# Optimization experiments

Measured on AMD Instinct MI355X. Metric: run time of the kernel, lower is better.

## Reference

```python
import jax, jax.numpy as jnp
from jax import lax
import numpy as np


def conv2d(x, w, b=None, stride=1, padding=0, groups=1, dilation=1):
    out = lax.conv_general_dilated(
        x, w, (stride, stride), [(padding, padding)] * 2,
        rhs_dilation=(dilation, dilation), feature_group_count=groups,
        dimension_numbers=('NCHW', 'OIHW', 'NCHW'))
    return out if b is None else out + b[None, :, None, None]


def unfold1d(x, k, axis):
    # torch.nn.functional.unfold with kernel (k,1) or (1,k), pad k//2 on that axis.
    # Returns [B, C, k, H, W] (channel-major, kernel-tap inner), matching torch layout.
    pad = k // 2
    pads = [(0, 0)] * 4
    pads[axis] = (pad, pad)
    xp = jnp.pad(x, pads)
    return jnp.stack([lax.slice_in_dim(xp, i, i + x.shape[axis], axis=axis)
                      for i in range(k)], axis=2)


def ikba(x, att, k, g, b_cb, w_cb):
    # Per-pixel dynamic grouped conv: attention mixes nset codebook kernels,
    # applied as vertical (k,1) then horizontal (1,k) unfold-matmul-fold.
    B, c, H, W = x.shape
    nset = att.shape[1]
    cg = c // g
    P = H * W
    a = att.reshape(B, nset, P).transpose(0, 2, 1)          # [B,P,nset]
    bias = a @ b_cb[0]                                      # [B,P,c]
    attk = a @ w_cb[0]                                      # [B,P, 2*c*cg*k]
    half = attk.shape[-1] // 2
    ah = attk[..., :half].reshape(B, P, g, cg, cg * k)
    aw = attk[..., half:].reshape(B, P, g, cg, cg * k)
    # vertical pass
    ufh = unfold1d(x, k, 2).reshape(B, g, cg * k, P).transpose(0, 3, 1, 2)  # [B,P,g,cg*k]
    xh = jnp.einsum('bpgij,bpgj->bpgi', ah, ufh).reshape(B, P, c)
    xh = xh.transpose(0, 2, 1).reshape(B, c, H, W)
    # horizontal pass
    ufw = unfold1d(xh, k, 3).reshape(B, g, cg * k, P).transpose(0, 3, 1, 2)
    xw = jnp.einsum('bpgij,bpgj->bpgi', aw, ufw).reshape(B, P, c) + bias
    return xw.transpose(0, 2, 1).reshape(B, c, H, W)


def hff_forward(x, dw1_w, dw2_w, proj_w, lka0_w, lkas_w, lka1_w, lka1_b,
                sca_w, sca_b, c1a_w, c1b_w, c2a_w, c2a_b, c2b_w, c2b_b,
                c211_w, c211_b, w_cb, b_cb, attgamma, ga1):
    C = x.shape[1]
    K, GC = 3, 4
    g = C // GC
    sca = conv2d(jnp.mean(x, axis=(2, 3), keepdims=True), sca_w, sca_b)
    x1 = conv2d(conv2d(x, dw1_w), dw2_w, padding=1, groups=C)
    lka = conv2d(conv2d(conv2d(x, lka0_w, padding=2, groups=C),
                        lkas_w, padding=9, groups=C, dilation=3), lka1_w, lka1_b)
    t = conv2d(x, c2a_w, c2a_b, padding=1, groups=c2a_w.shape[0])
    t1, t2 = jnp.split(t, 2, axis=1)  # SimpleGate
    att = conv2d(t1 * t2, c2b_w, c2b_b) * attgamma + conv2d(x, c211_w, c211_b)
    uf = conv2d(conv2d(x, c1a_w), c1b_w, padding=1, groups=C)
    x2 = ikba(uf, att, K, g, b_cb, w_cb) * ga1 + uf
    return conv2d(x1 * x2 * sca * lka, proj_w)


def setup_inputs() -> dict:
    key = jax.random.key(0)
    ks = jax.random.split(key, 24)
    B, C, H, W = 2, 256, 64, 64
    nset, k, gc = 128, 3, 4
    g = C // gc
    cg = C // g
    def rn(i, shape, scale=0.02):
        return jax.random.normal(ks[i], shape, jnp.float32) * scale
    return {
        'x': jax.random.normal(ks[0], (B, C, H, W), jnp.float32),
        'dw1_w': rn(1, (C, C, 1, 1)),
        'dw2_w': rn(2, (C, 1, 3, 3), 0.1),
        'proj_w': rn(3, (C, C, 1, 1)),
        'lka0_w': rn(4, (C, 1, 5, 5), 0.1),
        'lkas_w': rn(5, (C, 1, 7, 7), 0.1),
        'lka1_w': rn(6, (C, C, 1, 1)),
        'lka1_b': rn(7, (C,)),
        'sca_w': rn(8, (C, C, 1, 1)),
        'sca_b': rn(9, (C,)),
        'c1a_w': rn(10, (C, C, 1, 1)),
        'c1b_w': rn(11, (C, 1, 3, 3), 0.1),
        'c2a_w': rn(12, (32, C // 32, 3, 3), 0.1),
        'c2a_b': rn(13, (32,)),
        'c2b_w': rn(14, (nset, 16, 1, 1), 0.1),
        'c2b_b': rn(15, (nset,)),
        'c211_w': rn(16, (nset, C, 1, 1)),
        'c211_b': rn(17, (nset,)),
        'w_cb': rn(18, (1, nset, C * cg * k * 2), 0.05),
        'b_cb': rn(19, (1, nset, C), 0.05),
        'attgamma': jnp.full((1, nset, 1, 1), 0.01, jnp.float32),
        'ga1': jnp.full((1, C, 1, 1), 0.01, jnp.float32),
    }


def reference(x, dw1_w, dw2_w, proj_w, lka0_w, lkas_w, lka1_w, lka1_b,
              sca_w, sca_b, c1a_w, c1b_w, c2a_w, c2a_b, c2b_w, c2b_b,
              c211_w, c211_b, w_cb, b_cb, attgamma, ga1):
    return hff_forward(x, dw1_w, dw2_w, proj_w, lka0_w, lkas_w, lka1_w, lka1_b,
                       sca_w, sca_b, c1a_w, c1b_w, c2a_w, c2a_b, c2b_w, c2b_b,
                       c211_w, c211_b, w_cb, b_cb, attgamma, ga1)
```

## Files before the change

### kernel.cpp

```cpp
#include <hip/hip_runtime.h>
#include <cstddef>

#define P_ 4096
#define HW_ 64

typedef __bf16 bf16x8 __attribute__((ext_vector_type(8)));
typedef float f32x4 __attribute__((ext_vector_type(4)));

__device__ inline ushort f2bf(float f) {
  unsigned u = __float_as_uint(f);
  unsigned r = (u + 0x7FFFu + ((u >> 16) & 1u)) >> 16;
  return (ushort)r;
}
__device__ inline float bf2f(ushort h) {
  return __uint_as_float(((unsigned)h) << 16);
}
__device__ inline unsigned pack2(ushort a, ushort b) {
  return (unsigned)a | ((unsigned)b << 16);
}

__global__ __launch_bounds__(256) void prep_mean_kernel(
    const float* __restrict__ w_cb, const float* __restrict__ dw1_w,
    const float* __restrict__ lka1_w, const float* __restrict__ c1a_w,
    const float* __restrict__ proj_w, const float* __restrict__ c211_w,
    const float* __restrict__ b_cb, ushort* __restrict__ wT,
    ushort* __restrict__ W5h, ushort* __restrict__ W5l,
    ushort* __restrict__ bth, ushort* __restrict__ btl,
    const float* __restrict__ x, float* __restrict__ mean) {
  __shared__ float T[128][65];
  int blk = blockIdx.x;
  int t = threadIdx.x;
  if (blk < 96) {
    int c0 = blk * 64;
#pragma unroll
    for (int i = 0; i < 32; ++i) {
      int l = i * 256 + t;
      int n = l >> 6, c = l & 63;
      T[n][c] = w_cb[(size_t)n * 6144 + c0 + c];
    }
    __syncthreads();
#pragma unroll
    for (int i = 0; i < 4; ++i) {
      int l = i * 256 + t;
      int c = l >> 4, n8 = (l & 15) << 3;
      ushort v[8];
#pragma unroll
      for (int u = 0; u < 8; ++u) v[u] = f2bf(T[n8 + u][c]);
      *(uint4*)&wT[(size_t)(c0 + c) * 128 + n8] = *(uint4*)v;
    }
  } else if (blk < 240) {
    int f = (blk - 96) * 2048 + t * 8;
    const float* srcs[5] = {dw1_w, lka1_w, c1a_w, proj_w, c211_w};
    const int base[6] = {0, 65536, 131072, 196608, 262144, 294912};
    int r = 0;
    while (f >= base[r + 1]) ++r;
    const float* s = srcs[r] + (f - base[r]);
    float4 a = *(const float4*)s;
    float4 b4 = *(const float4*)(s + 4);
    float vv[8] = {a.x, a.y, a.z, a.w, b4.x, b4.y, b4.z, b4.w};
    ushort vh[8], vl[8];
#pragma unroll
    for (int u = 0; u < 8; ++u) {
      ushort h = f2bf(vv[u]);
      vh[u] = h;
      vl[u] = f2bf(vv[u] - bf2f(h));
    }
    *(uint4*)&W5h[f] = *(uint4*)vh;
    *(uint4*)&W5l[f] = *(uint4*)vl;
  } else if (blk < 244) {
    int c0 = (blk - 240) * 64;
#pragma unroll
    for (int i = 0; i < 32; ++i) {
      int l = i * 256 + t;
      int n = l >> 6, c = l & 63;
      T[n][c] = b_cb[(size_t)n * 256 + c0 + c];
    }
    __syncthreads();
#pragma unroll
    for (int i = 0; i < 4; ++i) {
      int l = i * 256 + t;
      int c = l >> 4, n8 = (l & 15) << 3;
      ushort vh[8], vl[8];
#pragma unroll
      for (int u = 0; u < 8; ++u) {
        float fv = T[n8 + u][c];
        ushort h = f2bf(fv);
        vh[u] = h;
        vl[u] = f2bf(fv - bf2f(h));
      }
      *(uint4*)&bth[(size_t)(c0 + c) * 128 + n8] = *(uint4*)vh;
      *(uint4*)&btl[(size_t)(c0 + c) * 128 + n8] = *(uint4*)vl;
    }
  } else {
    int bc = blk - 244;
    const float* xp = x + (size_t)bc * P_;
    float s = 0.f;
    for (int i = t; i < P_; i += 256) s += xp[i];
    float* red = (float*)T;
    red[t] = s;
    __syncthreads();
    for (int off2 = 128; off2 > 0; off2 >>= 1) {
      if (t < off2) red[t] += red[t + off2];
      __syncthreads();
    }
    if (t == 0) mean[bc] = red[0] * (1.f / P_);
  }
}

__global__ __launch_bounds__(256) void sca_xsplit_kernel(
    const float* __restrict__ x, ushort* __restrict__ dh,
    ushort* __restrict__ dl, const float* __restrict__ mean,
    const float* __restrict__ w, const float* __restrict__ bias,
    float* __restrict__ sca) {
  __shared__ float T[128][65];
  int blk = blockIdx.x;
  int t = threadIdx.x;
  if (blk < 256) {
    const int K = 256;
    int p0 = (blk & 63) * 64;
    int kb = (blk >> 6) & 1;
    int b = blk >> 7;
    const float* sb = x + ((size_t)b * K + kb * 128) * P_;
    ushort* dhb = dh + (size_t)b * P_ * K + (size_t)kb * 128;
    ushort* dlb = dl + (size_t)b * P_ * K + (size_t)kb * 128;
#pragma unroll
    for (int i = 0; i < 32; ++i) {
      int l = i * 256 + t;
      int n = l >> 6, c = l & 63;
      T[n][c] = sb[(size_t)n * P_ + p0 + c];
    }
    __syncthreads();
#pragma unroll
    for (int i = 0; i < 4; ++i) {
      int l = i * 256 + t;
      int c = l >> 4, n8 = (l & 15) << 3;
      ushort vh[8], vl[8];
#pragma unroll
      for (int u = 0; u < 8; ++u) {
        float f = T[n8 + u][c];
        ushort h = f2bf(f);
        vh[u] = h;
        vl[u] = f2bf(f - bf2f(h));
      }
      *(uint4*)&dhb[(size_t)(p0 + c) * K + n8] = *(uint4*)vh;
      *(uint4*)&dlb[(size_t)(p0 + c) * K + n8] = *(uint4*)vl;
    }
  } else {
    int b = blk - 256, c = t;
    const float* mb = mean + b * 256;
    const float* wr = w + c * 256;
    float s = bias[c];
    for (int k = 0; k < 256; ++k) s += wr[k] * mb[k];
    sca[b * 256 + c] = s;
  }
}

__global__ __launch_bounds__(256) void xsplit_kernel(
    const float* __restrict__ src, ushort* __restrict__ dh,
    ushort* __restrict__ dl, int K) {
  int p0 = blockIdx.x * 64;
  int kb = blockIdx.y;
  int b = blockIdx.z;
  const float* sb = src + ((size_t)b * K + kb * 128) * P_;
  ushort* dhb = dh + (size_t)b * P_ * K + (size_t)kb * 128;
  ushort* dlb = dl + (size_t)b * P_ * K + (size_t)kb * 128;
  __shared__ float T[128][65];
  int t = threadIdx.x;
#pragma unroll
  for (int i = 0; i < 32; ++i) {
    int l = i * 256 + t;
    int n = l >> 6, c = l & 63;
    T[n][c] = sb[(size_t)n * P_ + p0 + c];
  }
  __syncthreads();
#pragma unroll
  for (int i = 0; i < 4; ++i) {
    int l = i * 256 + t;
    int c = l >> 4, n8 = (l & 15) << 3;
    ushort vh[8], vl[8];
#pragma unroll
    for (int u = 0; u < 8; ++u) {
      float f = T[n8 + u][c];
      ushort h = f2bf(f);
      vh[u] = h;
      vl[u] = f2bf(f - bf2f(h));
    }
    *(uint4*)&dhb[(size_t)(p0 + c) * K + n8] = *(uint4*)vh;
    *(uint4*)&dlb[(size_t)(p0 + c) * K + n8] = *(uint4*)vl;
  }
}

__global__ __launch_bounds__(256) void gemm_bf16s_kernel(
    const ushort* __restrict__ Wh, const ushort* __restrict__ Wl,
    const ushort* __restrict__ Xh, const ushort* __restrict__ Xl,
    const float* __restrict__ bias, float* __restrict__ out, int M, int K) {
  int p0 = blockIdx.x * 64, m0 = blockIdx.y * 64, b = blockIdx.z;
  __shared__ __align__(16) ushort Wsh[64 * 72];
  __shared__ __align__(16) ushort Wsl[64 * 72];
  __shared__ __align__(16) ushort Xsh[64 * 72];
  __shared__ __align__(16) ushort Xsl[64 * 72];
  int t = threadIdx.x;
  int w = t >> 6, lane = t & 63, lm = lane & 15, lq = lane >> 4;
  f32x4 C[4];
#pragma unroll
  for (int pt = 0; pt < 4; ++pt) C[pt] = (f32x4)(0.f);
  const ushort* Whb = Wh + (size_t)m0 * K;
  const ushort* Wlb = Wl + (size_t)m0 * K;
  const ushort* Xhb = Xh + ((size_t)b * P_ + p0) * K;
  const ushort* Xlb = Xl + ((size_t)b * P_ + p0) * K;
  for (int k0 = 0; k0 < K; k0 += 64) {
#pragma unroll
    for (int i = 0; i < 2; ++i) {
      int u = i * 256 + t;
      int row = u >> 3, k8 = (u & 7) * 8;
      *(uint4*)&Wsh[row * 72 + k8] = *(const uint4*)&Whb[(size_t)row * K + k0 + k8];
      *(uint4*)&Wsl[row * 72 + k8] = *(const uint4*)&Wlb[(size_t)row * K + k0 + k8];
      *(uint4*)&Xsh[row * 72 + k8] = *(const uint4*)&Xhb[(size_t)row * K + k0 + k8];
      *(uint4*)&Xsl[row * 72 + k8] = *(const uint4*)&Xlb[(size_t)row * K + k0 + k8];
    }
    __syncthreads();
#pragma unroll
    for (int kt = 0; kt < 2; ++kt) {
      bf16x8 Ah = *(const bf16x8*)&Wsh[(w * 16 + lm) * 72 + kt * 32 + lq * 8];
      bf16x8 Al = *(const bf16x8*)&Wsl[(w * 16 + lm) * 72 + kt * 32 + lq * 8];
#pragma unroll
      for (int pt = 0; pt < 4; ++pt) {
        bf16x8 Bh = *(const bf16x8*)&Xsh[(pt * 16 + lm) * 72 + kt * 32 + lq * 8];
        bf16x8 Bl = *(const bf16x8*)&Xsl[(pt * 16 + lm) * 72 + kt * 32 + lq * 8];
        C[pt] = __builtin_amdgcn_mfma_f32_16x16x32_bf16(Ah, Bh, C[pt], 0, 0, 0);
        C[pt] = __builtin_amdgcn_mfma_f32_16x16x32_bf16(Al, Bh, C[pt], 0, 0, 0);
        C[pt] = __builtin_amdgcn_mfma_f32_16x16x32_bf16(Ah, Bl, C[pt], 0, 0, 0);
      }
    }
    __syncthreads();
  }
#pragma unroll
  for (int pt = 0; pt < 4; ++pt) {
    int p = p0 + pt * 16 + lm;
#pragma unroll
    for (int r = 0; r < 4; ++r) {
      int m = m0 + w * 16 + lq * 4 + r;
      float v = C[pt][r];
      if (bias) v += bias[m];
      out[((size_t)b * M + m) * P_ + p] = v;
    }
  }
}

__global__ __launch_bounds__(256) void gemm3_kernel(
    const ushort* __restrict__ Xh, const ushort* __restrict__ Xl,
    const ushort* __restrict__ W5h, const ushort* __restrict__ W5l,
    const float* __restrict__ c211_b, float* __restrict__ B1,
    float* __restrict__ B3, float* __restrict__ att0) {
  const int K = 256;
  int my = blockIdx.y;
  const ushort *Wh, *Wl;
  float* out;
  const float* bias = nullptr;
  int M, m0;
  if (my < 4) {
    Wh = W5h; Wl = W5l; out = B1; M = 256; m0 = my * 64;
  } else if (my < 8) {
    Wh = W5h + 131072; Wl = W5l + 131072; out = B3; M = 256; m0 = (my - 4) * 64;
  } else {
    Wh = W5h + 262144; Wl = W5l + 262144; out = att0; M = 128;
    m0 = (my - 8) * 64; bias = c211_b;
  }
  int p0 = blockIdx.x * 64, b = blockIdx.z;
  __shared__ __align__(16) ushort Wsh[64 * 72];
  __shared__ __align__(16) ushort Wsl[64 * 72];
  __shared__ __align__(16) ushort Xsh[64 * 72];
  __shared__ __align__(16) ushort Xsl[64 * 72];
  int t = threadIdx.x;
  int w = t >> 6, lane = t & 63, lm = lane & 15, lq = lane >> 4;
  f32x4 C[4];
#pragma unroll
  for (int pt = 0; pt < 4; ++pt) C[pt] = (f32x4)(0.f);
  const ushort* Whb = Wh + (size_t)m0 * K;
  const ushort* Wlb = Wl + (size_t)m0 * K;
  const ushort* Xhb = Xh + ((size_t)b * P_ + p0) * K;
  const ushort* Xlb = Xl + ((size_t)b * P_ + p0) * K;
  for (int k0 = 0; k0 < K; k0 += 64) {
#pragma unroll
    for (int i = 0; i < 2; ++i) {
      int u = i * 256 + t;
      int row = u >> 3, k8 = (u & 7) * 8;
      *(uint4*)&Wsh[row * 72 + k8] = *(const uint4*)&Whb[(size_t)row * K + k0 + k8];
      *(uint4*)&Wsl[row * 72 + k8] = *(const uint4*)&Wlb[(size_t)row * K + k0 + k8];
      *(uint4*)&Xsh[row * 72 + k8] = *(const uint4*)&Xhb[(size_t)row * K + k0 + k8];
      *(uint4*)&Xsl[row * 72 + k8] = *(const uint4*)&Xlb[(size_t)row * K + k0 + k8];
    }
    __syncthreads();
#pragma unroll
    for (int kt = 0; kt < 2; ++kt) {
      bf16x8 Ah = *(const bf16x8*)&Wsh[(w * 16 + lm) * 72 + kt * 32 + lq * 8];
      bf16x8 Al = *(const bf16x8*)&Wsl[(w * 16 + lm) * 72 + kt * 32 + lq * 8];
#pragma unroll
      for (int pt = 0; pt < 4; ++pt) {
        bf16x8 Bh = *(const bf16x8*)&Xsh[(pt * 16 + lm) * 72 + kt * 32 + lq * 8];
        bf16x8 Bl = *(const bf16x8*)&Xsl[(pt * 16 + lm) * 72 + kt * 32 + lq * 8];
        C[pt] = __builtin_amdgcn_mfma_f32_16x16x32_bf16(Ah, Bh, C[pt], 0, 0, 0);
        C[pt] = __builtin_amdgcn_mfma_f32_16x16x32_bf16(Al, Bh, C[pt], 0, 0, 0);
        C[pt] = __builtin_amdgcn_mfma_f32_16x16x32_bf16(Ah, Bl, C[pt], 0, 0, 0);
      }
    }
    __syncthreads();
  }
#pragma unroll
  for (int pt = 0; pt < 4; ++pt) {
    int p = p0 + pt * 16 + lm;
#pragma unroll
    for (int r = 0; r < 4; ++r) {
      int m = m0 + w * 16 + lq * 4 + r;
      float v = C[pt][r];
      if (bias) v += bias[m];
      out[((size_t)b * M + m) * P_ + p] = v;
    }
  }
}

__global__ __launch_bounds__(256) void lka_c2a_kernel(
    const float* __restrict__ in, const float* __restrict__ w0,
    const float* __restrict__ w1, float* __restrict__ outlka,
    const float* __restrict__ c2aw, const float* __restrict__ c2ab,
    float* __restrict__ sgate) {
  constexpr int PN0 = 68;
  constexpr int PN1 = 82;
  __shared__ float p0[PN0 * PN0];
  __shared__ float p1[PN1 * PN1];
  int t = threadIdx.x;
  if (blockIdx.x < 512) {
    int bc = blockIdx.x;
    const float* ib = in + (size_t)bc * P_;
    for (int i = t; i < PN0 * PN0; i += 256) p0[i] = 0.f;
    for (int i = t; i < PN1 * PN1; i += 256) p1[i] = 0.f;
    __syncthreads();
#pragma unroll
    for (int i = 0; i < 4; ++i) {
      int l = i * 1024 + t * 4;
      int y = l >> 6, xx = l & 63;
      float4 v = *(const float4*)(ib + l);
      float* d = &p0[(y + 2) * PN0 + 2 + xx];
      d[0] = v.x; d[1] = v.y; d[2] = v.z; d[3] = v.w;
    }
    float wr0[25];
    {
      const float* wp = w0 + (size_t)(bc & 255) * 25;
#pragma unroll
      for (int i = 0; i < 25; ++i) wr0[i] = wp[i];
    }
    __syncthreads();
#pragma unroll
    for (int r = 0; r < 16; ++r) {
      int l = r * 256 + t;
      int y = l >> 6, xx = l & 63;
      float s = 0.f;
#pragma unroll
      for (int dy = 0; dy < 5; ++dy)
#pragma unroll
        for (int dx = 0; dx < 5; ++dx)
          s += wr0[dy * 5 + dx] * p0[(y + dy) * PN0 + xx + dx];
      p1[(y + 9) * PN1 + 9 + xx] = s;
    }
    float wr1[49];
    {
      const float* wp = w1 + (size_t)(bc & 255) * 49;
#pragma unroll
      for (int i = 0; i < 49; ++i) wr1[i] = wp[i];
    }
    __syncthreads();
    float* ob = outlka + (size_t)bc * P_;
#pragma unroll
    for (int r = 0; r < 16; ++r) {
      int l = r * 256 + t;
      int y = l >> 6, xx = l & 63;
      float s = 0.f;
#pragma unroll
      for (int dy = 0; dy < 7; ++dy)
#pragma unroll
        for (int dx = 0; dx < 7; ++dx)
          s += wr1[dy * 7 + dx] * p1[(y + dy * 3) * PN1 + xx + dx * 3];
      ob[l] = s;
    }
  } else {
    int idx = (blockIdx.x - 512) * 256 + t;
    int xq = idx & 63, y = (idx >> 6) & 63, go = (idx >> 12) & 15, b = idx >> 16;
    float acc[2];
#pragma unroll
    for (int h = 0; h < 2; ++h) {
      int gc = go + h * 16;
      const float* wr = c2aw + gc * 72;
      const float* xb = in + ((size_t)b * 256 + gc * 8) * P_;
      float ss = c2ab[gc];
      for (int ci = 0; ci < 8; ++ci)
        for (int dy = 0; dy < 3; ++dy) {
          int yy = y + dy - 1;
          if (yy < 0 || yy >= 64) continue;
          for (int dx = 0; dx < 3; ++dx) {
            int xx = xq + dx - 1;
            if (xx < 0 || xx >= 64) continue;
            ss += wr[ci * 9 + dy * 3 + dx] * xb[(size_t)ci * P_ + yy * 64 + xx];
          }
        }
      acc[h] = ss;
    }
    sgate[idx] = acc[0] * acc[1];
  }
}

__global__ __launch_bounds__(256) void dw2x_kernel(
    const float* __restrict__ in1, const float* __restrict__ w1,
    float* __restrict__ out1, const float* __restrict__ in2,
    const float* __restrict__ w2, float* __restrict__ out2) {
  constexpr int PN = 66;
  __shared__ float pl[PN * PN];
  int which = blockIdx.x >> 9;
  int bc = blockIdx.x & 511;
  const float* in = which ? in2 : in1;
  const float* w = which ? w2 : w1;
  float* out = which ? out2 : out1;
  int t = threadIdx.x;
  const float* ib = in + (size_t)bc * P_;
  for (int i = t; i < PN * PN; i += 256) pl[i] = 0.f;
  __syncthreads();
#pragma unroll
  for (int i = 0; i < 4; ++i) {
    int l = i * 1024 + t * 4;
    int y = l >> 6, xx = l & 63;
    float4 v = *(const float4*)(ib + l);
    float* d = &pl[(y + 1) * PN + 1 + xx];
    d[0] = v.x; d[1] = v.y; d[2] = v.z; d[3] = v.w;
  }
  float wr[9];
  const float* wp = w + (size_t)(bc & 255) * 9;
#pragma unroll
  for (int i = 0; i < 9; ++i) wr[i] = wp[i];
  __syncthreads();
  float* ob = out + (size_t)bc * P_;
#pragma unroll
  for (int r = 0; r < 16; ++r) {
    int l = r * 256 + t;
    int y = l >> 6, xx = l & 63;
    float s = 0.f;
#pragma unroll
    for (int dy = 0; dy < 3; ++dy)
#pragma unroll
      for (int dx = 0; dx < 3; ++dx)
        s += wr[dy * 3 + dx] * pl[(y + dy) * PN + xx + dx];
    ob[l] = s;
  }
}

__global__ __launch_bounds__(256) void c2b_t_kernel(
    const float* __restrict__ in, const float* __restrict__ W,
    const float* __restrict__ bias, const float* __restrict__ gamma,
    const float* __restrict__ res, ushort* __restrict__ outh,
    ushort* __restrict__ outl) {
  const int K = 16, M = 128;
  int p0 = blockIdx.x * 64;
  int m0 = blockIdx.y * 64;
  int b  = blockIdx.z;
  __shared__ float Ws[16][68];
  __shared__ float Xs[16][68];
  int tid = threadIdx.x;
  int tm = tid >> 4, tp = tid & 15;
  float acc[4][4] = {};
  const float* inb = in + (size_t)b * K * P_;
  {
    int kk = tid >> 4, pq = (tid & 15) << 2;
    float4 v = *(const float4*)(inb + (size_t)kk * P_ + p0 + pq);
    *(float4*)&Xs[kk][pq] = v;
  }
  {
    int mm = tid >> 2, kq = (tid & 3) << 2;
    float4 v = *(const float4*)(W + (size_t)(m0 + mm) * K + kq);
    Ws[kq + 0][mm] = v.x; Ws[kq + 1][mm] = v.y;
    Ws[kq + 2][mm] = v.z; Ws[kq + 3][mm] = v.w;
  }
  __syncthreads();
#pragma unroll
  for (int kk = 0; kk < 16; ++kk) {
    const float4 wv = *(const float4*)&Ws[kk][tm << 2];
    const float4 xv = *(const float4*)&Xs[kk][tp << 2];
    const float wa[4] = {wv.x, wv.y, wv.z, wv.w};
    const float xa[4] = {xv.x, xv.y, xv.z, xv.w};
#pragma unroll
    for (int i = 0; i < 4; ++i)
#pragma unroll
      for (int j = 0; j < 4; ++j) acc[i][j] += wa[i] * xa[j];
  }
  float val[4][4];
#pragma unroll
  for (int i = 0; i < 4; ++i) {
    int m = m0 + (tm << 2) + i;
    float bv = bias[m], gm = gamma[m];
    float4 rv = *(const float4*)(res + ((size_t)b * M + m) * P_ + p0 + (tp << 2));
    val[i][0] = (acc[i][0] + bv) * gm + rv.x;
    val[i][1] = (acc[i][1] + bv) * gm + rv.y;
    val[i][2] = (acc[i][2] + bv) * gm + rv.z;
    val[i][3] = (acc[i][3] + bv) * gm + rv.w;
  }
#pragma unroll
  for (int j = 0; j < 4; ++j) {
    int p = p0 + (tp << 2) + j;
    ushort vh[4], vl[4];
#pragma unroll
    for (int i = 0; i < 4; ++i) {
      float f = val[i][j];
      ushort h = f2bf(f);
      vh[i] = h;
      vl[i] = f2bf(f - bf2f(h));
    }
    size_t a = ((size_t)b * P_ + p) * 128 + m0 + (tm << 2);
    uint2 hv, lv;
    hv.x = pack2(vh[0], vh[1]); hv.y = pack2(vh[2], vh[3]);
    lv.x = pack2(vl[0], vl[1]); lv.y = pack2(vl[2], vl[3]);
    *(uint2*)&outh[a] = hv;
    *(uint2*)&outl[a] = lv;
  }
}

__global__ __launch_bounds__(256) void ikba_mfma_kernel(
    const float* __restrict__ in, const ushort* __restrict__ attT,
    const ushort* __restrict__ Wt, int dirH, int wofs,
    const ushort* __restrict__ bth, const ushort* __restrict__ btl,
    const float* __restrict__ uf_ep, const float* __restrict__ ga1,
    const float* __restrict__ x1, const float* __restrict__ lka,
    const float* __restrict__ sca, ushort* __restrict__ pXh,
    ushort* __restrict__ pXl, float* __restrict__ outV) {
  __shared__ __align__(16) char smem[70656];
  ushort* Ws = (ushort*)smem;
  ushort* As = (ushort*)(smem + 53248);
  float*  Ts = (float*)smem;
  float*  ufs = (float*)(smem + 53248);
  float*  bls = (float*)(smem + 65536);

  int t = threadIdx.x;
  int b = blockIdx.z;
  int quad = blockIdx.y;
  int y = blockIdx.x;
  int p0 = y * 64;

  const ushort* Wg = Wt + ((size_t)wofs + (size_t)quad * 192) * 128;
  const ushort* Ab = attT + ((size_t)b * P_ + p0) * 128;
#pragma unroll
  for (int i = 0; i < 12; ++i) {
    int l = i * 256 + t;
    int c = l >> 4, n8 = (l & 15) << 3;
    *(uint4*)&Ws[c * 136 + n8] = *(const uint4*)&Wg[c * 128 + n8];
  }
#pragma unroll
  for (int i = 0; i < 4; ++i) {
    int l = i * 256 + t;
    int pp = l >> 4, n8 = (l & 15) << 3;
    *(uint4*)&As[pp * 136 + n8] = *(const uint4*)&Ab[pp * 128 + n8];
  }
  __syncthreads();

  int gg = t >> 6;
  int lane = t & 63;
  int lm = lane & 15, lq = lane >> 4;

  bf16x8 Af[3][4];
#pragma unroll
  for (int ct = 0; ct < 3; ++ct)
#pragma unroll
    for (int K = 0; K < 4; ++K)
      Af[ct][K] = *reinterpret_cast<const bf16x8*>(
          &Ws[(gg * 48 + ct * 16 + lm) * 136 + K * 32 + lq * 8]);

  f32x4 Cf[3][4];
#pragma unroll
  for (int ct = 0; ct < 3; ++ct)
#pragma unroll
    for (int pt = 0; pt < 4; ++pt) Cf[ct][pt] = (f32x4)(0.f);

#pragma unroll
  for (int pt = 0; pt < 4; ++pt) {
    bf16x8 Bf[4];
#pragma unroll
    for (int K = 0; K < 4; ++K)
      Bf[K] = *reinterpret_cast<const bf16x8*>(
          &As[(pt * 16 + lm) * 136 + K * 32 + lq * 8]);
#pragma unroll
    for (int ct = 0; ct < 3; ++ct)
#pragma unroll
      for (int K = 0; K < 4; ++K)
        Cf[ct][pt] = __builtin_amdgcn_mfma_f32_16x16x32_bf16(
            Af[ct][K], Bf[K], Cf[ct][pt], 0, 0, 0);
  }

  f32x4 Cb = (f32x4)(0.f);
  if (dirH) {
#pragma unroll
    for (int K = 0; K < 4; ++K) {
      bf16x8 Bb = *reinterpret_cast<const bf16x8*>(
          &As[(gg * 16 + lm) * 136 + K * 32 + lq * 8]);
      bf16x8 Abh = *(const bf16x8*)&bth[(size_t)(quad * 16 + lm) * 128 + K * 32 + lq * 8];
      bf16x8 Abl = *(const bf16x8*)&btl[(size_t)(quad * 16 + lm) * 128 + K * 32 + lq * 8];
      Cb = __builtin_amdgcn_mfma_f32_16x16x32_bf16(Abh, Bb, Cb, 0, 0, 0);
      Cb = __builtin_amdgcn_mfma_f32_16x16x32_bf16(Abl, Bb, Cb, 0, 0, 0);
    }
  }
  __syncthreads();

#pragma unroll
  for (int ct = 0; ct < 3; ++ct)
#pragma unroll
    for (int pt = 0; pt < 4; ++pt) {
      float* dst = &Ts[(gg * 64 + pt * 16 + lm) * 52 + ct * 16 + lq * 4];
      *(float4*)dst = *(float4*)&Cf[ct][pt];
    }
  if (dirH) {
    *(float4*)&bls[(gg * 16 + lm) * 16 + lq * 4] = *(float4*)&Cb;
  }
#pragma unroll
  for (int i = 0; i < 12; ++i) {
    int l = i * 256 + t;
    int chl = l >> 6, x = l & 63;
    int g2 = chl / 12, rem = chl % 12;
    int cj = rem / 3, tap = rem % 3;
    int ch = (quad * 4 + g2) * 4 + cj;
    float v = 0.f;
    if (dirH) {
      int xx = x + tap - 1;
      if (xx >= 0 && xx < 64) v = in[((size_t)b * 256 + ch) * P_ + p0 + xx];
    } else {
      int yy = y + tap - 1;
      if (yy >= 0 && yy < 64) v = in[((size_t)b * 256 + ch) * P_ + yy * 64 + x];
    }
    ufs[l] = v;
  }
  __syncthreads();

  int x = t & 63;
  int g2 = t >> 6;
  float u[12];
#pragma unroll
  for (int j = 0; j < 12; ++j) u[j] = ufs[(g2 * 12 + j) * 64 + x];
  const float* Tp = &Ts[(g2 * 64 + x) * 52];
  ushort vh[4], vl[4];
#pragma unroll
  for (int i = 0; i < 4; ++i) {
    float4 a0 = *(const float4*)&Tp[i * 12 + 0];
    float4 a1 = *(const float4*)&Tp[i * 12 + 4];
    float4 a2 = *(const float4*)&Tp[i * 12 + 8];
    float s = a0.x * u[0] + a0.y * u[1] + a0.z * u[2] + a0.w * u[3]
            + a1.x * u[4] + a1.y * u[5] + a1.z * u[6] + a1.w * u[7]
            + a2.x * u[8] + a2.y * u[9] + a2.z * u[10] + a2.w * u[11];
    int ch = (quad * 4 + g2) * 4 + i;
    size_t oidx = ((size_t)b * 256 + ch) * P_ + p0 + x;
    if (dirH) {
      float biasv = bls[x * 16 + g2 * 4 + i];
      float x2 = (s + biasv) * ga1[ch] + uf_ep[oidx];
      float pr = x1[oidx] * x2 * sca[b * 256 + ch] * lka[oidx];
      ushort h = f2bf(pr);
      vh[i] = h;
      vl[i] = f2bf(pr - bf2f(h));
    } else {
      outV[oidx] = s;
    }
  }
  if (dirH) {
    size_t xa = ((size_t)b * P_ + p0 + x) * 256 + quad * 16 + g2 * 4;
    uint2 hv, lv;
    hv.x = pack2(vh[0], vh[1]); hv.y = pack2(vh[2], vh[3]);
    lv.x = pack2(vl[0], vl[1]); lv.y = pack2(vl[2], vl[3]);
    *(uint2*)&pXh[xa] = hv;
    *(uint2*)&pXl[xa] = lv;
  }
}

extern "C" void kernel_launch(void* const* d_in, const int* in_sizes, int n_in,
                              void* d_out, int out_size, void* d_ws, size_t ws_size,
                              hipStream_t stream) {
  const float* x      = (const float*)d_in[0];
  const float* dw1_w  = (const float*)d_in[1];
  const float* dw2_w  = (const float*)d_in[2];
  const float* proj_w = (const float*)d_in[3];
  const float* lka0_w = (const float*)d_in[4];
  const float* lkas_w = (const float*)d_in[5];
  const float* lka1_w = (const float*)d_in[6];
  const float* lka1_b = (const float*)d_in[7];
  const float* sca_w  = (const float*)d_in[8];
  const float* sca_b  = (const float*)d_in[9];
  const float* c1a_w  = (const float*)d_in[10];
  const float* c1b_w  = (const float*)d_in[11];
  const float* c2a_w  = (const float*)d_in[12];
  const float* c2a_b  = (const float*)d_in[13];
  const float* c2b_w  = (const float*)d_in[14];
  const float* c2b_b  = (const float*)d_in[15];
  const float* c211_w = (const float*)d_in[16];
  const float* c211_b = (const float*)d_in[17];
  const float* w_cb   = (const float*)d_in[18];
  const float* b_cb   = (const float*)d_in[19];
  const float* attg   = (const float*)d_in[20];
  const float* ga1    = (const float*)d_in[21];
  float* out = (float*)d_out;

  const size_t NCHW = 2u * 256u * P_;
  float* ws = (float*)d_ws;
  size_t off = 0;
  float* meanb = ws + off; off += 512;
  float* scab  = ws + off; off += 512;
  float* B1 = ws + off; off += NCHW;
  float* B2 = ws + off; off += NCHW;
  float* B3 = ws + off; off += NCHW;
  float* B4 = ws + off; off += NCHW;
  float* B5 = ws + off; off += NCHW;
  float* B6 = ws + off; off += NCHW;
  float* sb   = ws + off; off += 2u * 16u * P_;
  float* att0 = ws + off; off += 2u * 128u * P_;
  ushort* wT    = (ushort*)(ws + off); off += 393216;
  ushort* W5h   = (ushort*)(ws + off); off += 147456;
  ushort* W5l   = (ushort*)(ws + off); off += 147456;
  ushort* bth   = (ushort*)(ws + off); off += 16384;
  ushort* btl   = (ushort*)(ws + off); off += 16384;
  ushort* XTxh  = (ushort*)(ws + off); off += 1048576;
  ushort* XTxl  = (ushort*)(ws + off); off += 1048576;
  ushort* XT2h  = (ushort*)(ws + off); off += 1048576;
  ushort* XT2l  = (ushort*)(ws + off); off += 1048576;
  ushort* XT3h  = (ushort*)(ws + off); off += 1048576;
  ushort* XT3l  = (ushort*)(ws + off); off += 1048576;
  ushort* attTh = (ushort*)(ws + off); off += 524288;
  ushort* attTl = (ushort*)(ws + off); off += 524288;

  const ushort* Wlka1h = W5h + 65536,  *Wlka1l = W5l + 65536;
  const ushort* Wprojh = W5h + 196608, *Wprojl = W5l + 196608;

  dim3 blk(256);

  prep_mean_kernel<<<756, blk, 0, stream>>>(w_cb, dw1_w, lka1_w, c1a_w, proj_w,
                                            c211_w, b_cb, wT, W5h, W5l, bth, btl,
                                            x, meanb);
  sca_xsplit_kernel<<<258, blk, 0, stream>>>(x, XTxh, XTxl, meanb, sca_w, sca_b,
                                             scab);
  gemm3_kernel<<<dim3(64, 10, 2), blk, 0, stream>>>(XTxh, XTxl, W5h, W5l, c211_b,
                                                    B1, B3, att0);
  lka_c2a_kernel<<<1024, blk, 0, stream>>>(x, lka0_w, lkas_w, B6, c2a_w, c2a_b, sb);
  dw2x_kernel<<<1024, blk, 0, stream>>>(B1, dw2_w, B2, B3, c1b_w, B5);
  xsplit_kernel<<<dim3(64, 2, 2), blk, 0, stream>>>(B6, XT2h, XT2l, 256);
  gemm_bf16s_kernel<<<dim3(64, 4, 2), blk, 0, stream>>>(Wlka1h, Wlka1l, XT2h,
                                                        XT2l, lka1_b, B1, 256, 256);
  c2b_t_kernel<<<dim3(64, 2, 2), blk, 0, stream>>>(sb, c2b_w, c2b_b, attg, att0,
                                                   attTh, attTl);
  dim3 gik(64, 16, 2);
  ikba_mfma_kernel<<<gik, blk, 0, stream>>>(B5, attTh, wT, 0, 0, nullptr, nullptr,
                                            nullptr, nullptr, nullptr, nullptr,
                                            nullptr, nullptr, nullptr, B4);
  ikba_mfma_kernel<<<gik, blk, 0, stream>>>(B4, attTh, wT, 1, 3072, bth, btl,
                                            B5, ga1, B2, B1, scab, XT3h, XT3l,
                                            nullptr);
  gemm_bf16s_kernel<<<dim3(64, 4, 2), blk, 0, stream>>>(Wprojh, Wprojl, XT3h,
                                                        XT3l, nullptr, out, 256, 256);
}
```

Measured before the change: 273.2 us.

## Merge independent stages into combined kernels and restructure ikba epilogue staging

```diff
diff --git a/kernel.cpp b/kernel.cpp
--- a/kernel.cpp
+++ b/kernel.cpp
@@ -107,12 +107,104 @@
   }
 }
 
+
+__device__ inline void xsplit_body(const float* sb, ushort* dhb, ushort* dlb,
+                                   int p0, int K, char* smem) {
+  float (*T)[65] = (float(*)[65])smem;
+  int t = threadIdx.x;
+#pragma unroll
+  for (int i = 0; i < 32; ++i) {
+    int l = i * 256 + t;
+    int n = l >> 6, c = l & 63;
+    T[n][c] = sb[(size_t)n * P_ + p0 + c];
+  }
+  __syncthreads();
+#pragma unroll
+  for (int i = 0; i < 4; ++i) {
+    int l = i * 256 + t;
+    int c = l >> 4, n8 = (l & 15) << 3;
+    ushort vh[8], vl[8];
+#pragma unroll
+    for (int u = 0; u < 8; ++u) {
+      float f = T[n8 + u][c];
+      ushort h = f2bf(f);
+      vh[u] = h;
+      vl[u] = f2bf(f - bf2f(h));
+    }
+    *(uint4*)&dhb[(size_t)(p0 + c) * K + n8] = *(uint4*)vh;
+    *(uint4*)&dlb[(size_t)(p0 + c) * K + n8] = *(uint4*)vl;
+  }
+}
+
+__device__ inline void gemm_body(const ushort* Whb, const ushort* Wlb,
+                                 const ushort* Xhb, const ushort* Xlb,
+                                 const float* bias, float* out, int M, int m0,
+                                 int p0, int b, int K, char* smem) {
+  ushort* Wsh = (ushort*)smem;
+  ushort* Wsl = (ushort*)(smem + 9216);
+  ushort* Xsh = (ushort*)(smem + 18432);
+  ushort* Xsl = (ushort*)(smem + 27648);
+  int t = threadIdx.x;
+  int w = t >> 6, lane = t & 63, lm = lane & 15, lq = lane >> 4;
+  f32x4 C[4];
+#pragma unroll
+  for (int pt = 0; pt < 4; ++pt) C[pt] = (f32x4)(0.f);
+  for (int k0 = 0; k0 < K; k0 += 64) {
+#pragma unroll
+    for (int i = 0; i < 2; ++i) {
+      int u = i * 256 + t;
+      int row = u >> 3, k8 = (u & 7) * 8;
+      *(uint4*)&Wsh[row * 72 + k8] = *(const uint4*)&Whb[(size_t)row * K + k0 + k8];
+      *(uint4*)&Wsl[row * 72 + k8] = *(const uint4*)&Wlb[(size_t)row * K + k0 + k8];
+      *(uint4*)&Xsh[row * 72 + k8] = *(const uint4*)&Xhb[(size_t)row * K + k0 + k8];
+      *(uint4*)&Xsl[row * 72 + k8] = *(const uint4*)&Xlb[(size_t)row * K + k0 + k8];
+    }
+    __syncthreads();
+#pragma unroll
+    for (int kt = 0; kt < 2; ++kt) {
+      bf16x8 Ah = *(const bf16x8*)&Wsh[(w * 16 + lm) * 72 + kt * 32 + lq * 8];
+      bf16x8 Al = *(const bf16x8*)&Wsl[(w * 16 + lm) * 72 + kt * 32 + lq * 8];
+#pragma unroll
+      for (int pt = 0; pt < 4; ++pt) {
+        bf16x8 Bh = *(const bf16x8*)&Xsh[(pt * 16 + lm) * 72 + kt * 32 + lq * 8];
+        bf16x8 Bl = *(const bf16x8*)&Xsl[(pt * 16 + lm) * 72 + kt * 32 + lq * 8];
+        C[pt] = __builtin_amdgcn_mfma_f32_16x16x32_bf16(Ah, Bh, C[pt], 0, 0, 0);
+        C[pt] = __builtin_amdgcn_mfma_f32_16x16x32_bf16(Al, Bh, C[pt], 0, 0, 0);
+        C[pt] = __builtin_amdgcn_mfma_f32_16x16x32_bf16(Ah, Bl, C[pt], 0, 0, 0);
+      }
+    }
+    __syncthreads();
+  }
+#pragma unroll
+  for (int pt = 0; pt < 4; ++pt) {
+    int p = p0 + pt * 16 + lm;
+#pragma unroll
+    for (int r = 0; r < 4; ++r) {
+      int m = m0 + w * 16 + lq * 4 + r;
+      float v = C[pt][r];
+      if (bias) v += bias[m];
+      out[((size_t)b * M + m) * P_ + p] = v;
+    }
+  }
+}
+
+__global__ __launch_bounds__(256) void gemm_bf16s_kernel(
+    const ushort* __restrict__ Wh, const ushort* __restrict__ Wl,
+    const ushort* __restrict__ Xh, const ushort* __restrict__ Xl,
+    const float* __restrict__ bias, float* __restrict__ out, int M, int K) {
+  __shared__ __align__(16) char smem[36864];
+  int p0 = blockIdx.x * 64, m0 = blockIdx.y * 64, b = blockIdx.z;
+  gemm_body(Wh + (size_t)m0 * K, Wl + (size_t)m0 * K,
+            Xh + ((size_t)b * P_ + p0) * K, Xl + ((size_t)b * P_ + p0) * K,
+            bias, out, M, m0, p0, b, K, smem);
+}
+
 __global__ __launch_bounds__(256) void sca_xsplit_kernel(
     const float* __restrict__ x, ushort* __restrict__ dh,
     ushort* __restrict__ dl, const float* __restrict__ mean,
     const float* __restrict__ w, const float* __restrict__ bias,
     float* __restrict__ sca) {
-  __shared__ float T[128][65];
+  __shared__ __align__(16) char smem[33280];
   int blk = blockIdx.x;
   int t = threadIdx.x;
   if (blk < 256) {
@@ -120,31 +212,9 @@
     int p0 = (blk & 63) * 64;
     int kb = (blk >> 6) & 1;
     int b = blk >> 7;
-    const float* sb = x + ((size_t)b * K + kb * 128) * P_;
-    ushort* dhb = dh + (size_t)b * P_ * K + (size_t)kb * 128;
-    ushort* dlb = dl + (size_t)b * P_ * K + (size_t)kb * 128;
-#pragma unroll
-    for (int i = 0; i < 32; ++i) {
-      int l = i * 256 + t;
-      int n = l >> 6, c = l & 63;
-      T[n][c] = sb[(size_t)n * P_ + p0 + c];
-    }
-    __syncthreads();
-#pragma unroll
-    for (int i = 0; i < 4; ++i) {
-      int l = i * 256 + t;
-      int c = l >> 4, n8 = (l & 15) << 3;
-      ushort vh[8], vl[8];
-#pragma unroll
-      for (int u = 0; u < 8; ++u) {
-        float f = T[n8 + u][c];
-        ushort h = f2bf(f);
-        vh[u] = h;
-        vl[u] = f2bf(f - bf2f(h));
-      }
-      *(uint4*)&dhb[(size_t)(p0 + c) * K + n8] = *(uint4*)vh;
-      *(uint4*)&dlb[(size_t)(p0 + c) * K + n8] = *(uint4*)vl;
-    }
+    xsplit_body(x + ((size_t)b * K + kb * 128) * P_,
+                dh + (size_t)b * P_ * K + (size_t)kb * 128,
+                dl + (size_t)b * P_ * K + (size_t)kb * 128, p0, K, smem);
   } else {
     int b = blk - 256, c = t;
     const float* mb = mean + b * 256;
@@ -155,192 +225,55 @@
   }
 }
 
-__global__ __launch_bounds__(256) void xsplit_kernel(
-    const float* __restrict__ src, ushort* __restrict__ dh,
-    ushort* __restrict__ dl, int K) {
-  int p0 = blockIdx.x * 64;
-  int kb = blockIdx.y;
-  int b = blockIdx.z;
-  const float* sb = src + ((size_t)b * K + kb * 128) * P_;
-  ushort* dhb = dh + (size_t)b * P_ * K + (size_t)kb * 128;
-  ushort* dlb = dl + (size_t)b * P_ * K + (size_t)kb * 128;
-  __shared__ float T[128][65];
-  int t = threadIdx.x;
-#pragma unroll
-  for (int i = 0; i < 32; ++i) {
-    int l = i * 256 + t;
-    int n = l >> 6, c = l & 63;
-    T[n][c] = sb[(size_t)n * P_ + p0 + c];
-  }
-  __syncthreads();
-#pragma unroll
-  for (int i = 0; i < 4; ++i) {
-    int l = i * 256 + t;
-    int c = l >> 4, n8 = (l & 15) << 3;
-    ushort vh[8], vl[8];
-#pragma unroll
-    for (int u = 0; u < 8; ++u) {
-      float f = T[n8 + u][c];
-      ushort h = f2bf(f);
-      vh[u] = h;
-      vl[u] = f2bf(f - bf2f(h));
-    }
-    *(uint4*)&dhb[(size_t)(p0 + c) * K + n8] = *(uint4*)vh;
-    *(uint4*)&dlb[(size_t)(p0 + c) * K + n8] = *(uint4*)vl;
-  }
-}
-
-__global__ __launch_bounds__(256) void gemm_bf16s_kernel(
-    const ushort* __restrict__ Wh, const ushort* __restrict__ Wl,
-    const ushort* __restrict__ Xh, const ushort* __restrict__ Xl,
-    const float* __restrict__ bias, float* __restrict__ out, int M, int K) {
-  int p0 = blockIdx.x * 64, m0 = blockIdx.y * 64, b = blockIdx.z;
-  __shared__ __align__(16) ushort Wsh[64 * 72];
-  __shared__ __align__(16) ushort Wsl[64 * 72];
-  __shared__ __align__(16) ushort Xsh[64 * 72];
-  __shared__ __align__(16) ushort Xsl[64 * 72];
-  int t = threadIdx.x;
-  int w = t >> 6, lane = t & 63, lm = lane & 15, lq = lane >> 4;
-  f32x4 C[4];
-#pragma unroll
-  for (int pt = 0; pt < 4; ++pt) C[pt] = (f32x4)(0.f);
-  const ushort* Whb = Wh + (size_t)m0 * K;
-  const ushort* Wlb = Wl + (size_t)m0 * K;
-  const ushort* Xhb = Xh + ((size_t)b * P_ + p0) * K;
-  const ushort* Xlb = Xl + ((size_t)b * P_ + p0) * K;
-  for (int k0 = 0; k0 < K; k0 += 64) {
-#pragma unroll
-    for (int i = 0; i < 2; ++i) {
-      int u = i * 256 + t;
-      int row = u >> 3, k8 = (u & 7) * 8;
-      *(uint4*)&Wsh[row * 72 + k8] = *(const uint4*)&Whb[(size_t)row * K + k0 + k8];
-      *(uint4*)&Wsl[row * 72 + k8] = *(const uint4*)&Wlb[(size_t)row * K + k0 + k8];
-      *(uint4*)&Xsh[row * 72 + k8] = *(const uint4*)&Xhb[(size_t)row * K + k0 + k8];
-      *(uint4*)&Xsl[row * 72 + k8] = *(const uint4*)&Xlb[(size_t)row * K + k0 + k8];
-    }
-    __syncthreads();
-#pragma unroll
-    for (int kt = 0; kt < 2; ++kt) {
-      bf16x8 Ah = *(const bf16x8*)&Wsh[(w * 16 + lm) * 72 + kt * 32 + lq * 8];
-      bf16x8 Al = *(const bf16x8*)&Wsl[(w * 16 + lm) * 72 + kt * 32 + lq * 8];
-#pragma unroll
-      for (int pt = 0; pt < 4; ++pt) {
-        bf16x8 Bh = *(const bf16x8*)&Xsh[(pt * 16 + lm) * 72 + kt * 32 + lq * 8];
-        bf16x8 Bl = *(const bf16x8*)&Xsl[(pt * 16 + lm) * 72 + kt * 32 + lq * 8];
-        C[pt] = __builtin_amdgcn_mfma_f32_16x16x32_bf16(Ah, Bh, C[pt], 0, 0, 0);
-        C[pt] = __builtin_amdgcn_mfma_f32_16x16x32_bf16(Al, Bh, C[pt], 0, 0, 0);
-        C[pt] = __builtin_amdgcn_mfma_f32_16x16x32_bf16(Ah, Bl, C[pt], 0, 0, 0);
-      }
-    }
-    __syncthreads();
-  }
-#pragma unroll
-  for (int pt = 0; pt < 4; ++pt) {
-    int p = p0 + pt * 16 + lm;
-#pragma unroll
-    for (int r = 0; r < 4; ++r) {
-      int m = m0 + w * 16 + lq * 4 + r;
-      float v = C[pt][r];
-      if (bias) v += bias[m];
-      out[((size_t)b * M + m) * P_ + p] = v;
-    }
-  }
-}
-
-__global__ __launch_bounds__(256) void gemm3_kernel(
+__global__ __launch_bounds__(256) void main1_kernel(
     const ushort* __restrict__ Xh, const ushort* __restrict__ Xl,
     const ushort* __restrict__ W5h, const ushort* __restrict__ W5l,
     const float* __restrict__ c211_b, float* __restrict__ B1,
-    float* __restrict__ B3, float* __restrict__ att0) {
-  const int K = 256;
-  int my = blockIdx.y;
-  const ushort *Wh, *Wl;
-  float* out;
-  const float* bias = nullptr;
-  int M, m0;
-  if (my < 4) {
-    Wh = W5h; Wl = W5l; out = B1; M = 256; m0 = my * 64;
-  } else if (my < 8) {
-    Wh = W5h + 131072; Wl = W5l + 131072; out = B3; M = 256; m0 = (my - 4) * 64;
-  } else {
-    Wh = W5h + 262144; Wl = W5l + 262144; out = att0; M = 128;
-    m0 = (my - 8) * 64; bias = c211_b;
-  }
-  int p0 = blockIdx.x * 64, b = blockIdx.z;
-  __shared__ __align__(16) ushort Wsh[64 * 72];
-  __shared__ __align__(16) ushort Wsl[64 * 72];
-  __shared__ __align__(16) ushort Xsh[64 * 72];
-  __shared__ __align__(16) ushort Xsl[64 * 72];
-  int t = threadIdx.x;
-  int w = t >> 6, lane = t & 63, lm = lane & 15, lq = lane >> 4;
-  f32x4 C[4];
-#pragma unroll
-  for (int pt = 0; pt < 4; ++pt) C[pt] = (f32x4)(0.f);
-  const ushort* Whb = Wh + (size_t)m0 * K;
-  const ushort* Wlb = Wl + (size_t)m0 * K;
-  const ushort* Xhb = Xh + ((size_t)b * P_ + p0) * K;
-  const ushort* Xlb = Xl + ((size_t)b * P_ + p0) * K;
-  for (int k0 = 0; k0 < K; k0 += 64) {
-#pragma unroll
-    for (int i = 0; i < 2; ++i) {
-      int u = i * 256 + t;
-      int row = u >> 3, k8 = (u & 7) * 8;
-      *(uint4*)&Wsh[row * 72 + k8] = *(const uint4*)&Whb[(size_t)row * K + k0 + k8];
-      *(uint4*)&Wsl[row * 72 + k8] = *(const uint4*)&Wlb[(size_t)row * K + k0 + k8];
-      *(uint4*)&Xsh[row * 72 + k8] = *(const uint4*)&Xhb[(size_t)row * K + k0 + k8];
-      *(uint4*)&Xsl[row * 72 + k8] = *(const uint4*)&Xlb[(size_t)row * K + k0 + k8];
-    }
-    __syncthreads();
-#pragma unroll
-    for (int kt = 0; kt < 2; ++kt) {
-      bf16x8 Ah = *(const bf16x8*)&Wsh[(w * 16 + lm) * 72 + kt * 32 + lq * 8];
-      bf16x8 Al = *(const bf16x8*)&Wsl[(w * 16 + lm) * 72 + kt * 32 + lq * 8];
-#pragma unroll
-      for (int pt = 0; pt < 4; ++pt) {
-        bf16x8 Bh = *(const bf16x8*)&Xsh[(pt * 16 + lm) * 72 + kt * 32 + lq * 8];
-        bf16x8 Bl = *(const bf16x8*)&Xsl[(pt * 16 + lm) * 72 + kt * 32 + lq * 8];
-        C[pt] = __builtin_amdgcn_mfma_f32_16x16x32_bf16(Ah, Bh, C[pt], 0, 0, 0);
-        C[pt] = __builtin_amdgcn_mfma_f32_16x16x32_bf16(Al, Bh, C[pt], 0, 0, 0);
-        C[pt] = __builtin_amdgcn_mfma_f32_16x16x32_bf16(Ah, Bl, C[pt], 0, 0, 0);
-      }
-    }
-    __syncthreads();
-  }
-#pragma unroll
-  for (int pt = 0; pt < 4; ++pt) {
-    int p = p0 + pt * 16 + lm;
-#pragma unroll
-    for (int r = 0; r < 4; ++r) {
-      int m = m0 + w * 16 + lq * 4 + r;
-      float v = C[pt][r];
-      if (bias) v += bias[m];
-      out[((size_t)b * M + m) * P_ + p] = v;
-    }
-  }
-}
-
-__global__ __launch_bounds__(256) void lka_c2a_kernel(
-    const float* __restrict__ in, const float* __restrict__ w0,
+    float* __restrict__ B3, float* __restrict__ att0,
+    const float* __restrict__ x, const float* __restrict__ w0,
     const float* __restrict__ w1, float* __restrict__ outlka,
     const float* __restrict__ c2aw, const float* __restrict__ c2ab,
     float* __restrict__ sgate) {
-  constexpr int PN0 = 68;
-  constexpr int PN1 = 82;
-  __shared__ float p0[PN0 * PN0];
-  __shared__ float p1[PN1 * PN1];
-  int t = threadIdx.x;
-  if (blockIdx.x < 512) {
-    int bc = blockIdx.x;
-    const float* ib = in + (size_t)bc * P_;
-    for (int i = t; i < PN0 * PN0; i += 256) p0[i] = 0.f;
-    for (int i = t; i < PN1 * PN1; i += 256) p1[i] = 0.f;
+  __shared__ __align__(16) char smem[45392];
+  int blk = blockIdx.x;
+  int t = threadIdx.x;
+  if (blk < 1280) {
+    const int K = 256;
+    int p = blk & 63;
+    int my = (blk >> 6) % 10;
+    int b = blk / 640;
+    const ushort *Wh, *Wl;
+    float* out;
+    const float* bias = nullptr;
+    int M, m0;
+    if (my < 4) {
+      Wh = W5h; Wl = W5l; out = B1; M = 256; m0 = my * 64;
+    } else if (my < 8) {
+      Wh = W5h + 131072; Wl = W5l + 131072; out = B3; M = 256; m0 = (my - 4) * 64;
+    } else {
+      Wh = W5h + 262144; Wl = W5l + 262144; out = att0; M = 128;
+      m0 = (my - 8) * 64; bias = c211_b;
+    }
+    int p0 = p * 64;
+    gemm_body(Wh + (size_t)m0 * K, Wl + (size_t)m0 * K,
+              Xh + ((size_t)b * P_ + p0) * K, Xl + ((size_t)b * P_ + p0) * K,
+              bias, out, M, m0, p0, b, K, smem);
+  } else if (blk < 1792) {
+    constexpr int PN0 = 68;
+    constexpr int PN1 = 82;
+    float* p0a = (float*)smem;
+    float* p1a = (float*)(smem + PN0 * PN0 * 4);
+    int bc = blk - 1280;
+    const float* ib = x + (size_t)bc * P_;
+    for (int i = t; i < PN0 * PN0; i += 256) p0a[i] = 0.f;
+    for (int i = t; i < PN1 * PN1; i += 256) p1a[i] = 0.f;
     __syncthreads();
 #pragma unroll
     for (int i = 0; i < 4; ++i) {
       int l = i * 1024 + t * 4;
       int y = l >> 6, xx = l & 63;
       float4 v = *(const float4*)(ib + l);
-      float* d = &p0[(y + 2) * PN0 + 2 + xx];
+      float* d = &p0a[(y + 2) * PN0 + 2 + xx];
       d[0] = v.x; d[1] = v.y; d[2] = v.z; d[3] = v.w;
     }
     float wr0[25];
@@ -359,8 +292,8 @@
       for (int dy = 0; dy < 5; ++dy)
 #pragma unroll
         for (int dx = 0; dx < 5; ++dx)
-          s += wr0[dy * 5 + dx] * p0[(y + dy) * PN0 + xx + dx];
-      p1[(y + 9) * PN1 + 9 + xx] = s;
+          s += wr0[dy * 5 + dx] * p0a[(y + dy) * PN0 + xx + dx];
+      p1a[(y + 9) * PN1 + 9 + xx] = s;
     }
     float wr1[49];
     {
@@ -379,18 +312,18 @@
       for (int dy = 0; dy < 7; ++dy)
 #pragma unroll
         for (int dx = 0; dx < 7; ++dx)
-          s += wr1[dy * 7 + dx] * p1[(y + dy * 3) * PN1 + xx + dx * 3];
+          s += wr1[dy * 7 + dx] * p1a[(y + dy * 3) * PN1 + xx + dx * 3];
       ob[l] = s;
     }
   } else {
-    int idx = (blockIdx.x - 512) * 256 + t;
+    int idx = (blk - 1792) * 256 + t;
     int xq = idx & 63, y = (idx >> 6) & 63, go = (idx >> 12) & 15, b = idx >> 16;
     float acc[2];
 #pragma unroll
     for (int h = 0; h < 2; ++h) {
       int gc = go + h * 16;
       const float* wr = c2aw + gc * 72;
-      const float* xb = in + ((size_t)b * 256 + gc * 8) * P_;
+      const float* xb = x + ((size_t)b * 256 + gc * 8) * P_;
       float ss = c2ab[gc];
       for (int ci = 0; ci < 8; ++ci)
         for (int dy = 0; dy < 3; ++dy) {
@@ -408,115 +341,143 @@
   }
 }
 
-__global__ __launch_bounds__(256) void dw2x_kernel(
+__global__ __launch_bounds__(256) void dwsplit_kernel(
     const float* __restrict__ in1, const float* __restrict__ w1,
     float* __restrict__ out1, const float* __restrict__ in2,
-    const float* __restrict__ w2, float* __restrict__ out2) {
-  constexpr int PN = 66;
-  __shared__ float pl[PN * PN];
-  int which = blockIdx.x >> 9;
-  int bc = blockIdx.x & 511;
-  const float* in = which ? in2 : in1;
-  const float* w = which ? w2 : w1;
-  float* out = which ? out2 : out1;
-  int t = threadIdx.x;
-  const float* ib = in + (size_t)bc * P_;
-  for (int i = t; i < PN * PN; i += 256) pl[i] = 0.f;
-  __syncthreads();
-#pragma unroll
-  for (int i = 0; i < 4; ++i) {
-    int l = i * 1024 + t * 4;
-    int y = l >> 6, xx = l & 63;
-    float4 v = *(const float4*)(ib + l);
-    float* d = &pl[(y + 1) * PN + 1 + xx];
-    d[0] = v.x; d[1] = v.y; d[2] = v.z; d[3] = v.w;
-  }
-  float wr[9];
-  const float* wp = w + (size_t)(bc & 255) * 9;
-#pragma unroll
-  for (int i = 0; i < 9; ++i) wr[i] = wp[i];
-  __syncthreads();
-  float* ob = out + (size_t)bc * P_;
-#pragma unroll
-  for (int r = 0; r < 16; ++r) {
-    int l = r * 256 + t;
-    int y = l >> 6, xx = l & 63;
-    float s = 0.f;
-#pragma unroll
-    for (int dy = 0; dy < 3; ++dy)
-#pragma unroll
-      for (int dx = 0; dx < 3; ++dx)
-        s += wr[dy * 3 + dx] * pl[(y + dy) * PN + xx + dx];
-    ob[l] = s;
-  }
-}
-
-__global__ __launch_bounds__(256) void c2b_t_kernel(
-    const float* __restrict__ in, const float* __restrict__ W,
-    const float* __restrict__ bias, const float* __restrict__ gamma,
+    const float* __restrict__ w2, float* __restrict__ out2,
+    const float* __restrict__ B6, ushort* __restrict__ XT2h,
+    ushort* __restrict__ XT2l) {
+  __shared__ __align__(16) char smem[33280];
+  int blk = blockIdx.x;
+  int t = threadIdx.x;
+  if (blk < 1024) {
+    constexpr int PN = 66;
+    float* pl = (float*)smem;
+    int which = blk >> 9;
+    int bc = blk & 511;
+    const float* in = which ? in2 : in1;
+    const float* w = which ? w2 : w1;
+    float* out = which ? out2 : out1;
+    const float* ib = in + (size_t)bc * P_;
+    for (int i = t; i < PN * PN; i += 256) pl[i] = 0.f;
+    __syncthreads();
+#pragma unroll
+    for (int i = 0; i < 4; ++i) {
+      int l = i * 1024 + t * 4;
+      int y = l >> 6, xx = l & 63;
+      float4 v = *(const float4*)(ib + l);
+      float* d = &pl[(y + 1) * PN + 1 + xx];
+      d[0] = v.x; d[1] = v.y; d[2] = v.z; d[3] = v.w;
+    }
+    float wr[9];
+    const float* wp = w + (size_t)(bc & 255) * 9;
+#pragma unroll
+    for (int i = 0; i < 9; ++i) wr[i] = wp[i];
+    __syncthreads();
+    float* ob = out + (size_t)bc * P_;
+#pragma unroll
+    for (int r = 0; r < 16; ++r) {
+      int l = r * 256 + t;
+      int y = l >> 6, xx = l & 63;
+      float s = 0.f;
+#pragma unroll
+      for (int dy = 0; dy < 3; ++dy)
+#pragma unroll
+        for (int dx = 0; dx < 3; ++dx)
+          s += wr[dy * 3 + dx] * pl[(y + dy) * PN + xx + dx];
+      ob[l] = s;
+    }
+  } else {
+    const int K = 256;
+    int l = blk - 1024;
+    int p0 = (l & 63) * 64;
+    int kb = (l >> 6) & 1;
+    int b = l >> 7;
+    xsplit_body(B6 + ((size_t)b * K + kb * 128) * P_,
+                XT2h + (size_t)b * P_ * K + (size_t)kb * 128,
+                XT2l + (size_t)b * P_ * K + (size_t)kb * 128, p0, K, smem);
+  }
+}
+
+__global__ __launch_bounds__(256) void gemm_c2b_kernel(
+    const ushort* __restrict__ Wh, const ushort* __restrict__ Wl,
+    const ushort* __restrict__ XT2h, const ushort* __restrict__ XT2l,
+    const float* __restrict__ lka1_b, float* __restrict__ B1,
+    const float* __restrict__ sb, const float* __restrict__ c2bw,
+    const float* __restrict__ c2bb, const float* __restrict__ gamma,
     const float* __restrict__ res, ushort* __restrict__ outh,
     ushort* __restrict__ outl) {
-  const int K = 16, M = 128;
-  int p0 = blockIdx.x * 64;
-  int m0 = blockIdx.y * 64;
-  int b  = blockIdx.z;
-  __shared__ float Ws[16][68];
-  __shared__ float Xs[16][68];
-  int tid = threadIdx.x;
-  int tm = tid >> 4, tp = tid & 15;
-  float acc[4][4] = {};
-  const float* inb = in + (size_t)b * K * P_;
-  {
-    int kk = tid >> 4, pq = (tid & 15) << 2;
-    float4 v = *(const float4*)(inb + (size_t)kk * P_ + p0 + pq);
-    *(float4*)&Xs[kk][pq] = v;
-  }
-  {
-    int mm = tid >> 2, kq = (tid & 3) << 2;
-    float4 v = *(const float4*)(W + (size_t)(m0 + mm) * K + kq);
-    Ws[kq + 0][mm] = v.x; Ws[kq + 1][mm] = v.y;
-    Ws[kq + 2][mm] = v.z; Ws[kq + 3][mm] = v.w;
-  }
-  __syncthreads();
-#pragma unroll
-  for (int kk = 0; kk < 16; ++kk) {
-    const float4 wv = *(const float4*)&Ws[kk][tm << 2];
-    const float4 xv = *(const float4*)&Xs[kk][tp << 2];
-    const float wa[4] = {wv.x, wv.y, wv.z, wv.w};
-    const float xa[4] = {xv.x, xv.y, xv.z, xv.w};
-#pragma unroll
-    for (int i = 0; i < 4; ++i)
-#pragma unroll
-      for (int j = 0; j < 4; ++j) acc[i][j] += wa[i] * xa[j];
-  }
-  float val[4][4];
-#pragma unroll
-  for (int i = 0; i < 4; ++i) {
-    int m = m0 + (tm << 2) + i;
-    float bv = bias[m], gm = gamma[m];
-    float4 rv = *(const float4*)(res + ((size_t)b * M + m) * P_ + p0 + (tp << 2));
-    val[i][0] = (acc[i][0] + bv) * gm + rv.x;
-    val[i][1] = (acc[i][1] + bv) * gm + rv.y;
-    val[i][2] = (acc[i][2] + bv) * gm + rv.z;
-    val[i][3] = (acc[i][3] + bv) * gm + rv.w;
-  }
-#pragma unroll
-  for (int j = 0; j < 4; ++j) {
-    int p = p0 + (tp << 2) + j;
-    ushort vh[4], vl[4];
+  __shared__ __align__(16) char smem[36864];
+  int my = blockIdx.y;
+  int b = blockIdx.z;
+  int t = threadIdx.x;
+  if (my < 4) {
+    const int K = 256;
+    int p0 = blockIdx.x * 64, m0 = my * 64;
+    gemm_body(Wh + (size_t)m0 * K, Wl + (size_t)m0 * K,
+              XT2h + ((size_t)b * P_ + p0) * K, XT2l + ((size_t)b * P_ + p0) * K,
+              lka1_b, B1, 256, m0, p0, b, K, smem);
+  } else {
+    const int K = 16, M = 128;
+    int p0 = blockIdx.x * 64;
+    int m0 = (my - 4) * 64;
+    float (*Ws)[68] = (float(*)[68])smem;
+    float (*Xs)[68] = (float(*)[68])(smem + 4352 * 4);
+    int tm = t >> 4, tp = t & 15;
+    float acc[4][4] = {};
+    const float* inb = sb + (size_t)b * K * P_;
+    {
+      int kk = t >> 4, pq = (t & 15) << 2;
+      float4 v = *(const float4*)(inb + (size_t)kk * P_ + p0 + pq);
+      *(float4*)&Xs[kk][pq] = v;
+    }
+    {
+      int mm = t >> 2, kq = (t & 3) << 2;
+      float4 v = *(const float4*)(c2bw + (size_t)(m0 + mm) * K + kq);
+      Ws[kq + 0][mm] = v.x; Ws[kq + 1][mm] = v.y;
+      Ws[kq + 2][mm] = v.z; Ws[kq + 3][mm] = v.w;
+    }
+    __syncthreads();
+#pragma unroll
+    for (int kk = 0; kk < 16; ++kk) {
+      const float4 wv = *(const float4*)&Ws[kk][tm << 2];
+      const float4 xv = *(const float4*)&Xs[kk][tp << 2];
+      const float wa[4] = {wv.x, wv.y, wv.z, wv.w};
+      const float xa[4] = {xv.x, xv.y, xv.z, xv.w};
+#pragma unroll
+      for (int i = 0; i < 4; ++i)
+#pragma unroll
+        for (int j = 0; j < 4; ++j) acc[i][j] += wa[i] * xa[j];
+    }
+    float val[4][4];
 #pragma unroll
     for (int i = 0; i < 4; ++i) {
-      float f = val[i][j];
-      ushort h = f2bf(f);
-      vh[i] = h;
-      vl[i] = f2bf(f - bf2f(h));
-    }
-    size_t a = ((size_t)b * P_ + p) * 128 + m0 + (tm << 2);
-    uint2 hv, lv;
-    hv.x = pack2(vh[0], vh[1]); hv.y = pack2(vh[2], vh[3]);
-    lv.x = pack2(vl[0], vl[1]); lv.y = pack2(vl[2], vl[3]);
-    *(uint2*)&outh[a] = hv;
-    *(uint2*)&outl[a] = lv;
+      int m = m0 + (tm << 2) + i;
+      float bv = c2bb[m], gm = gamma[m];
+      float4 rv = *(const float4*)(res + ((size_t)b * M + m) * P_ + p0 + (tp << 2));
+      val[i][0] = (acc[i][0] + bv) * gm + rv.x;
+      val[i][1] = (acc[i][1] + bv) * gm + rv.y;
+      val[i][2] = (acc[i][2] + bv) * gm + rv.z;
+      val[i][3] = (acc[i][3] + bv) * gm + rv.w;
+    }
+#pragma unroll
+    for (int j = 0; j < 4; ++j) {
+      int p = p0 + (tp << 2) + j;
+      ushort vh[4], vl[4];
+#pragma unroll
+      for (int i = 0; i < 4; ++i) {
+        float f = val[i][j];
+        ushort h = f2bf(f);
+        vh[i] = h;
+        vl[i] = f2bf(f - bf2f(h));
+      }
+      size_t a = ((size_t)b * P_ + p) * 128 + m0 + (tm << 2);
+      uint2 hv, lv;
+      hv.x = pack2(vh[0], vh[1]); hv.y = pack2(vh[2], vh[3]);
+      lv.x = pack2(vl[0], vl[1]); lv.y = pack2(vl[2], vl[3]);
+      *(uint2*)&outh[a] = hv;
+      *(uint2*)&outl[a] = lv;
+    }
   }
 }
 
@@ -528,47 +489,29 @@
     const float* __restrict__ x1, const float* __restrict__ lka,
     const float* __restrict__ sca, ushort* __restrict__ pXh,
     ushort* __restrict__ pXl, float* __restrict__ outV) {
-  __shared__ __align__(16) char smem[70656];
-  ushort* Ws = (ushort*)smem;
-  ushort* As = (ushort*)(smem + 53248);
-  float*  Ts = (float*)smem;
-  float*  ufs = (float*)(smem + 53248);
-  float*  bls = (float*)(smem + 65536);
+  __shared__ float Ts[2][4][16][66];
+  __shared__ float bls[64 * 17];
 
   int t = threadIdx.x;
   int b = blockIdx.z;
   int quad = blockIdx.y;
   int y = blockIdx.x;
   int p0 = y * 64;
-
-  const ushort* Wg = Wt + ((size_t)wofs + (size_t)quad * 192) * 128;
-  const ushort* Ab = attT + ((size_t)b * P_ + p0) * 128;
-#pragma unroll
-  for (int i = 0; i < 12; ++i) {
-    int l = i * 256 + t;
-    int c = l >> 4, n8 = (l & 15) << 3;
-    *(uint4*)&Ws[c * 136 + n8] = *(const uint4*)&Wg[c * 128 + n8];
-  }
-#pragma unroll
-  for (int i = 0; i < 4; ++i) {
-    int l = i * 256 + t;
-    int pp = l >> 4, n8 = (l & 15) << 3;
-    *(uint4*)&As[pp * 136 + n8] = *(const uint4*)&Ab[pp * 128 + n8];
-  }
-  __syncthreads();
-
   int gg = t >> 6;
   int lane = t & 63;
   int lm = lane & 15, lq = lane >> 4;
-
+  int gi = quad * 4 + gg;
+  int x = lane;
+
+  const ushort* Wbase = Wt + ((size_t)wofs + (size_t)gi * 48) * 128;
   bf16x8 Af[3][4];
 #pragma unroll
   for (int ct = 0; ct < 3; ++ct)
 #pragma unroll
     for (int K = 0; K < 4; ++K)
-      Af[ct][K] = *reinterpret_cast<const bf16x8*>(
-          &Ws[(gg * 48 + ct * 16 + lm) * 136 + K * 32 + lq * 8]);
-
+      Af[ct][K] = *(const bf16x8*)&Wbase[(ct * 16 + lm) * 128 + K * 32 + lq * 8];
+
+  const ushort* Ab = attT + ((size_t)b * P_ + p0) * 128;
   f32x4 Cf[3][4];
 #pragma unroll
   for (int ct = 0; ct < 3; ++ct)
@@ -580,8 +523,7 @@
     bf16x8 Bf[4];
 #pragma unroll
     for (int K = 0; K < 4; ++K)
-      Bf[K] = *reinterpret_cast<const bf16x8*>(
-          &As[(pt * 16 + lm) * 136 + K * 32 + lq * 8]);
+      Bf[K] = *(const bf16x8*)&Ab[(pt * 16 + lm) * 128 + K * 32 + lq * 8];
 #pragma unroll
     for (int ct = 0; ct < 3; ++ct)
 #pragma unroll
@@ -590,82 +532,81 @@
             Af[ct][K], Bf[K], Cf[ct][pt], 0, 0, 0);
   }
 
-  f32x4 Cb = (f32x4)(0.f);
   if (dirH) {
+    f32x4 Cb = (f32x4)(0.f);
 #pragma unroll
     for (int K = 0; K < 4; ++K) {
-      bf16x8 Bb = *reinterpret_cast<const bf16x8*>(
-          &As[(gg * 16 + lm) * 136 + K * 32 + lq * 8]);
+      bf16x8 Bb = *(const bf16x8*)&Ab[(gg * 16 + lm) * 128 + K * 32 + lq * 8];
       bf16x8 Abh = *(const bf16x8*)&bth[(size_t)(quad * 16 + lm) * 128 + K * 32 + lq * 8];
       bf16x8 Abl = *(const bf16x8*)&btl[(size_t)(quad * 16 + lm) * 128 + K * 32 + lq * 8];
       Cb = __builtin_amdgcn_mfma_f32_16x16x32_bf16(Abh, Bb, Cb, 0, 0, 0);
       Cb = __builtin_amdgcn_mfma_f32_16x16x32_bf16(Abl, Bb, Cb, 0, 0, 0);
     }
-  }
-  __syncthreads();
-
-#pragma unroll
-  for (int ct = 0; ct < 3; ++ct)
-#pragma unroll
-    for (int pt = 0; pt < 4; ++pt) {
-      float* dst = &Ts[(gg * 64 + pt * 16 + lm) * 52 + ct * 16 + lq * 4];
-      *(float4*)dst = *(float4*)&Cf[ct][pt];
-    }
+#pragma unroll
+    for (int r = 0; r < 4; ++r)
+      bls[(gg * 16 + lm) * 17 + lq * 4 + r] = Cb[r];
+  }
+
+  float u[12];
+  const float* inb = in + ((size_t)b * 256 + gi * 4) * P_;
   if (dirH) {
-    *(float4*)&bls[(gg * 16 + lm) * 16 + lq * 4] = *(float4*)&Cb;
-  }
-#pragma unroll
-  for (int i = 0; i < 12; ++i) {
-    int l = i * 256 + t;
-    int chl = l >> 6, x = l & 63;
-    int g2 = chl / 12, rem = chl % 12;
-    int cj = rem / 3, tap = rem % 3;
-    int ch = (quad * 4 + g2) * 4 + cj;
-    float v = 0.f;
-    if (dirH) {
+#pragma unroll
+    for (int j = 0; j < 12; ++j) {
+      int ci = j / 3, tap = j % 3;
       int xx = x + tap - 1;
-      if (xx >= 0 && xx < 64) v = in[((size_t)b * 256 + ch) * P_ + p0 + xx];
-    } else {
+      u[j] = (xx >= 0 && xx < 64) ? inb[(size_t)ci * P_ + p0 + xx] : 0.f;
+    }
+  } else {
+#pragma unroll
+    for (int j = 0; j < 12; ++j) {
+      int ci = j / 3, tap = j % 3;
       int yy = y + tap - 1;
-      if (yy >= 0 && yy < 64) v = in[((size_t)b * 256 + ch) * P_ + yy * 64 + x];
-    }
-    ufs[l] = v;
-  }
-  __syncthreads();
-
-  int x = t & 63;
-  int g2 = t >> 6;
-  float u[12];
-#pragma unroll
-  for (int j = 0; j < 12; ++j) u[j] = ufs[(g2 * 12 + j) * 64 + x];
-  const float* Tp = &Ts[(g2 * 64 + x) * 52];
-  ushort vh[4], vl[4];
+      u[j] = (yy >= 0 && yy < 64) ? inb[(size_t)ci * P_ + yy * 64 + x] : 0.f;
+    }
+  }
+
+  float s4[4] = {0.f, 0.f, 0.f, 0.f};
+#pragma unroll
+  for (int ct = 0; ct < 3; ++ct) {
+    int bi = ct & 1;
+#pragma unroll
+    for (int pt = 0; pt < 4; ++pt)
+#pragma unroll
+      for (int r = 0; r < 4; ++r)
+        Ts[bi][gg][lq * 4 + r][pt * 16 + lm] = Cf[ct][pt][r];
+    __syncthreads();
+#pragma unroll
+    for (int cl = 0; cl < 16; ++cl) {
+      int col = ct * 16 + cl;
+      int i = col / 12, j = col % 12;
+      s4[i] += Ts[bi][gg][cl][x] * u[j];
+    }
+  }
+
 #pragma unroll
   for (int i = 0; i < 4; ++i) {
-    float4 a0 = *(const float4*)&Tp[i * 12 + 0];
-    float4 a1 = *(const float4*)&Tp[i * 12 + 4];
-    float4 a2 = *(const float4*)&Tp[i * 12 + 8];
-    float s = a0.x * u[0] + a0.y * u[1] + a0.z * u[2] + a0.w * u[3]
-            + a1.x * u[4] + a1.y * u[5] + a1.z * u[6] + a1.w * u[7]
-            + a2.x * u[8] + a2.y * u[9] + a2.z * u[10] + a2.w * u[11];
-    int ch = (quad * 4 + g2) * 4 + i;
+    int ch = gi * 4 + i;
     size_t oidx = ((size_t)b * 256 + ch) * P_ + p0 + x;
     if (dirH) {
-      float biasv = bls[x * 16 + g2 * 4 + i];
-      float x2 = (s + biasv) * ga1[ch] + uf_ep[oidx];
-      float pr = x1[oidx] * x2 * sca[b * 256 + ch] * lka[oidx];
+      float biasv = bls[x * 17 + gg * 4 + i];
+      float x2v = (s4[i] + biasv) * ga1[ch] + uf_ep[oidx];
+      float pr = x1[oidx] * x2v * sca[b * 256 + ch] * lka[oidx];
       ushort h = f2bf(pr);
-      vh[i] = h;
-      vl[i] = f2bf(pr - bf2f(h));
+      ushort lo = f2bf(pr - bf2f(h));
+      s4[i] = __uint_as_float(pack2(h, lo));
     } else {
-      outV[oidx] = s;
+      outV[oidx] = s4[i];
     }
   }
   if (dirH) {
-    size_t xa = ((size_t)b * P_ + p0 + x) * 256 + quad * 16 + g2 * 4;
+    size_t xa = ((size_t)b * P_ + p0 + x) * 256 + quad * 16 + gg * 4;
     uint2 hv, lv;
-    hv.x = pack2(vh[0], vh[1]); hv.y = pack2(vh[2], vh[3]);
-    lv.x = pack2(vl[0], vl[1]); lv.y = pack2(vl[2], vl[3]);
+    unsigned w0 = __float_as_uint(s4[0]), w1 = __float_as_uint(s4[1]);
+    unsigned w2 = __float_as_uint(s4[2]), w3 = __float_as_uint(s4[3]);
+    hv.x = (w0 & 0xFFFFu) | ((w1 & 0xFFFFu) << 16);
+    hv.y = (w2 & 0xFFFFu) | ((w3 & 0xFFFFu) << 16);
+    lv.x = (w0 >> 16) | (w1 & 0xFFFF0000u);
+    lv.y = (w2 >> 16) | (w3 & 0xFFFF0000u);
     *(uint2*)&pXh[xa] = hv;
     *(uint2*)&pXl[xa] = lv;
   }
@@ -735,15 +676,14 @@
                                             x, meanb);
   sca_xsplit_kernel<<<258, blk, 0, stream>>>(x, XTxh, XTxl, meanb, sca_w, sca_b,
                                              scab);
-  gemm3_kernel<<<dim3(64, 10, 2), blk, 0, stream>>>(XTxh, XTxl, W5h, W5l, c211_b,
-                                                    B1, B3, att0);
-  lka_c2a_kernel<<<1024, blk, 0, stream>>>(x, lka0_w, lkas_w, B6, c2a_w, c2a_b, sb);
-  dw2x_kernel<<<1024, blk, 0, stream>>>(B1, dw2_w, B2, B3, c1b_w, B5);
-  xsplit_kernel<<<dim3(64, 2, 2), blk, 0, stream>>>(B6, XT2h, XT2l, 256);
-  gemm_bf16s_kernel<<<dim3(64, 4, 2), blk, 0, stream>>>(Wlka1h, Wlka1l, XT2h,
-                                                        XT2l, lka1_b, B1, 256, 256);
-  c2b_t_kernel<<<dim3(64, 2, 2), blk, 0, stream>>>(sb, c2b_w, c2b_b, attg, att0,
-                                                   attTh, attTl);
+  main1_kernel<<<2304, blk, 0, stream>>>(XTxh, XTxl, W5h, W5l, c211_b,
+                                         B1, B3, att0, x, lka0_w, lkas_w, B6,
+                                         c2a_w, c2a_b, sb);
+  dwsplit_kernel<<<1280, blk, 0, stream>>>(B1, dw2_w, B2, B3, c1b_w, B5,
+                                           B6, XT2h, XT2l);
+  gemm_c2b_kernel<<<dim3(64, 6, 2), blk, 0, stream>>>(
+      Wlka1h, Wlka1l, XT2h, XT2l, lka1_b, B1,
+      sb, c2b_w, c2b_b, attg, att0, attTh, attTl);
   dim3 gik(64, 16, 2);
   ikba_mfma_kernel<<<gik, blk, 0, stream>>>(B5, attTh, wT, 0, 0, nullptr, nullptr,
                                             nullptr, nullptr, nullptr, nullptr,
```

Result: no change. 272.4 us (-0.3%).
